# Kernel optimization log

Measured on AMD Instinct MI355X. Metric: run time of the kernel, lower is better.

The kernel has to match this reference:

```python
import jax, jax.numpy as jnp
import numpy as np

B, H, W, C = 4, 64, 64, 1280
NH = 16          # num heads
HD = C // NH     # 80 features per head
WS = 14          # window size
REL = 2 * WS - 1 # 27 relative-position entries per axis
EPS = 1e-6


def setup_inputs() -> dict:
    key = jax.random.key(0)
    ks = jax.random.split(key, 16)
    s = 0.02
    return {
        "imagelike_bhwc": jax.random.normal(ks[0], (B, H, W, C), jnp.float32),
        "ln1_g": jnp.ones((C,), jnp.float32),
        "ln1_b": jnp.zeros((C,), jnp.float32),
        "qkv_w": jax.random.normal(ks[1], (C, 3 * C), jnp.float32) * s,
        "qkv_b": jnp.zeros((3 * C,), jnp.float32),
        "proj_w": jax.random.normal(ks[2], (C, C), jnp.float32) * s,
        "proj_b": jnp.zeros((C,), jnp.float32),
        "rel_pos_h": jax.random.normal(ks[3], (REL, HD), jnp.float32) * s,
        "rel_pos_w": jax.random.normal(ks[4], (REL, HD), jnp.float32) * s,
        "ln2_g": jnp.ones((C,), jnp.float32),
        "ln2_b": jnp.zeros((C,), jnp.float32),
        "mlp_w1": jax.random.normal(ks[5], (C, 4 * C), jnp.float32) * s,
        "mlp_b1": jnp.zeros((4 * C,), jnp.float32),
        "mlp_w2": jax.random.normal(ks[6], (4 * C, C), jnp.float32) * s,
        "mlp_b2": jnp.zeros((C,), jnp.float32),
    }


def _layernorm(t, g, b):
    mu = jnp.mean(t, axis=-1, keepdims=True)
    var = jnp.var(t, axis=-1, keepdims=True)
    return (t - mu) * jax.lax.rsqrt(var + EPS) * g + b


def reference(imagelike_bhwc, ln1_g, ln1_b, qkv_w, qkv_b, proj_w, proj_b,
              rel_pos_h, rel_pos_w, ln2_g, ln2_b, mlp_w1, mlp_b1, mlp_w2, mlp_b2):
    x = imagelike_bhwc
    b, h, w, c = x.shape
    hd = c // NH
    scale = hd ** -0.5
    # --- image -> windows (pad to multiple of WS) ---
    hp, wp = (-h) % WS, (-w) % WS
    xp = jnp.pad(x, ((0, 0), (0, hp), (0, wp), (0, 0)))
    Hp, Wp = h + hp, w + wp
    ny, nx = Hp // WS, Wp // WS
    win = xp.reshape(b, ny, WS, nx, WS, c).transpose(0, 1, 3, 2, 4, 5)
    win = win.reshape(b * ny * nx, WS, WS, c)      # (Bw, S, S, C)
    Bw, N = win.shape[0], WS * WS
    # --- pre-attention layernorm + qkv ---
    t = _layernorm(win, ln1_g, ln1_b)
    qkv = t.reshape(Bw, N, c) @ qkv_w + qkv_b      # (Bw, N, 3C)
    qkv = qkv.reshape(Bw, N, 3, NH, hd).transpose(2, 0, 3, 1, 4)  # (3,Bw,NH,N,hd)
    q, k, v = qkv[0], qkv[1], qkv[2]
    # --- scores + decomposed relative position bias ---
    attn = jnp.einsum('bhqd,bhkd->bhqk', q * scale, k)            # (Bw,NH,N,N)
    idx = jnp.arange(WS)[:, None] - jnp.arange(WS)[None, :] + (WS - 1)
    Rh = rel_pos_h[idx]                                           # (WS,WS,hd)
    Rw = rel_pos_w[idx]                                           # (WS,WS,hd)
    qr = q.reshape(Bw, NH, WS, WS, hd)
    bias_h = jnp.einsum('bnyxd,ykd->bnyxk', qr, Rh)               # (Bw,NH,WS,WS,WS)
    bias_w = jnp.einsum('bnyxd,xkd->bnyxk', qr, Rw)
    bias = (bias_h[..., :, None] + bias_w[..., None, :]).reshape(Bw, NH, N, N)
    attn = jax.nn.softmax(attn + bias, axis=-1)
    out = jnp.einsum('bhqk,bhkd->bhqd', attn, v)                  # (Bw,NH,N,hd)
    out = out.transpose(0, 2, 1, 3).reshape(Bw, WS, WS, c)
    out = out @ proj_w + proj_b
    attn_out = out + win                                          # residual 1
    # --- MLP ---
    t2 = _layernorm(attn_out, ln2_g, ln2_b)
    mlp = jax.nn.gelu(t2 @ mlp_w1 + mlp_b1, approximate=False) @ mlp_w2 + mlp_b2
    out = mlp + attn_out                                          # residual 2
    # --- windows -> image (remove padding) ---
    img = out.reshape(b, ny, nx, WS, WS, c).transpose(0, 1, 3, 2, 4, 5)
    img = img.reshape(b, Hp, Wp, c)
    return img[:, :h, :w, :]
```

## Files before the change

kernel.cpp:

```cpp
#include <hip/hip_runtime.h>

typedef __attribute__((ext_vector_type(8))) short short8;
typedef __attribute__((ext_vector_type(4))) float f32x4;

#define GLBP(p) ((const __attribute__((address_space(1))) void*)(p))
#define LDSP(p) ((__attribute__((address_space(3))) void*)(p))

__device__ __forceinline__ float bf2f(unsigned short u) {
  return __uint_as_float(((unsigned int)u) << 16);
}
__device__ __forceinline__ unsigned short f2bf(float f) {
  unsigned int u = __float_as_uint(f);
  u += 0x7fff + ((u >> 16) & 1);
  return (unsigned short)(u >> 16);
}

__device__ __forceinline__ void tok2pix(int gt, int& b, int& py, int& px) {
  int w = gt / 196, t = gt - w * 196;
  b = w / 25;
  int wr = w - b * 25;
  int wy = wr / 5, wx = wr - wy * 5;
  int ty = t / 14;
  py = wy * 14 + ty;
  px = wx * 14 + (t - ty * 14);
}

__global__ void k_transpose(const float* __restrict__ W, unsigned short* __restrict__ Wt,
                            int K, int N) {
  __shared__ float tile[32][33];
  int tx = threadIdx.x, ty = threadIdx.y;
  int n0 = blockIdx.x * 32, k0 = blockIdx.y * 32;
#pragma unroll
  for (int i = 0; i < 4; ++i)
    tile[ty + 8 * i][tx] = W[(size_t)(k0 + ty + 8 * i) * N + n0 + tx];
  __syncthreads();
#pragma unroll
  for (int i = 0; i < 4; ++i)
    Wt[(size_t)(n0 + ty + 8 * i) * K + k0 + tx] = f2bf(tile[tx][ty + 8 * i]);
}

__global__ __launch_bounds__(256) void k_ln1(const float* __restrict__ x,
                                             const float* __restrict__ g,
                                             const float* __restrict__ be,
                                             unsigned short* __restrict__ A1,
                                             int w0, int ctok) {
  int m = blockIdx.x, tid = threadIdx.x;
  int b, py, px;
  tok2pix(w0 * 196 + m, b, py, px);
  bool valid = (m < ctok) && (py < 64) && (px < 64);
  const float* row = x + ((size_t)((b * 64 + py) * 64 + px)) * 1280;
  float v[5];
#pragma unroll
  for (int i = 0; i < 5; ++i) v[i] = valid ? row[tid + 256 * i] : 0.f;
  float s = 0.f, ss = 0.f;
#pragma unroll
  for (int i = 0; i < 5; ++i) { s += v[i]; ss += v[i] * v[i]; }
#pragma unroll
  for (int o = 32; o > 0; o >>= 1) { s += __shfl_down(s, o); ss += __shfl_down(ss, o); }
  __shared__ float rs[8];
  int wid = tid >> 6, lane = tid & 63;
  if (lane == 0) { rs[wid] = s; rs[wid + 4] = ss; }
  __syncthreads();
  s = rs[0] + rs[1] + rs[2] + rs[3];
  ss = rs[4] + rs[5] + rs[6] + rs[7];
  float mu = s * (1.f / 1280.f);
  float var = ss * (1.f / 1280.f) - mu * mu;
  float rinv = rsqrtf(var + 1e-6f);
  unsigned short* o1 = A1 + (size_t)m * 1280;
#pragma unroll
  for (int i = 0; i < 5; ++i) {
    int c = tid + 256 * i;
    o1[c] = f2bf((v[i] - mu) * rinv * g[c] + be[c]);
  }
}

__global__ __launch_bounds__(256) void k_ln2(const unsigned short* __restrict__ AT,
                                             const float* __restrict__ g,
                                             const float* __restrict__ be,
                                             unsigned short* __restrict__ A2) {
  int m = blockIdx.x, tid = threadIdx.x;
  const unsigned short* row = AT + (size_t)m * 1280;
  float v[5];
#pragma unroll
  for (int i = 0; i < 5; ++i) v[i] = bf2f(row[tid + 256 * i]);
  float s = 0.f, ss = 0.f;
#pragma unroll
  for (int i = 0; i < 5; ++i) { s += v[i]; ss += v[i] * v[i]; }
#pragma unroll
  for (int o = 32; o > 0; o >>= 1) { s += __shfl_down(s, o); ss += __shfl_down(ss, o); }
  __shared__ float rs[8];
  int wid = tid >> 6, lane = tid & 63;
  if (lane == 0) { rs[wid] = s; rs[wid + 4] = ss; }
  __syncthreads();
  s = rs[0] + rs[1] + rs[2] + rs[3];
  ss = rs[4] + rs[5] + rs[6] + rs[7];
  float mu = s * (1.f / 1280.f);
  float var = ss * (1.f / 1280.f) - mu * mu;
  float rinv = rsqrtf(var + 1e-6f);
  unsigned short* o1 = A2 + (size_t)m * 1280;
#pragma unroll
  for (int i = 0; i < 5; ++i) {
    int c = tid + 256 * i;
    o1[c] = f2bf((v[i] - mu) * rinv * g[c] + be[c]);
  }
}

template <int EPI>
__global__ __launch_bounds__(512, 2) void k_gemm256(const unsigned short* __restrict__ A,
                                                    const unsigned short* __restrict__ Bt,
                                                    int K, int N, int gx,
                                                    const float* __restrict__ bias,
                                                    void* __restrict__ outp,
                                                    const float* __restrict__ xres,
                                                    const unsigned short* __restrict__ attnres,
                                                    int w0, int ctok) {
  __shared__ __align__(16) char smem[131072];
  int tid = threadIdx.x;
  int w = tid >> 6, lane = tid & 63;
  int nwg = gridDim.x, bid = blockIdx.x;
  int q = nwg >> 3, r = nwg & 7;
  int xcd = bid & 7, loc = bid >> 3;
  int wg = (xcd < r ? xcd * (q + 1) : r * (q + 1) + (xcd - r) * q) + loc;
  int bx = wg % gx, by = wg / gx;
  int mBase = by * 256, nBase = bx * 256;
  int wr = w >> 2, wc = w & 3;
  int la = lane & 15, lg = lane >> 4;

  int rS = w * 16 + (lane >> 2);
  int kbyte = (((lane & 3) ^ ((lane >> 3) & 3)) << 4);
  const char* Ab = (const char*)A;
  const char* Bb = (const char*)Bt;
  const char* pa0 = Ab + ((size_t)(mBase + rS) * K) * 2 + kbyte;
  const char* pa1 = Ab + ((size_t)(mBase + 128 + rS) * K) * 2 + kbyte;
  const char* pb0 = Bb + ((size_t)(nBase + rS) * K) * 2 + kbyte;
  const char* pb1 = Bb + ((size_t)(nBase + 128 + rS) * K) * 2 + kbyte;
  int ldsw = w * 1024;

  auto STAGE = [&](int t) {
    int b = (t & 3) * 32768;
    size_t ko = (size_t)t * 64;
    __builtin_amdgcn_global_load_lds(GLBP(pa0 + ko), LDSP(smem + b + ldsw), 16, 0, 0);
    __builtin_amdgcn_global_load_lds(GLBP(pa1 + ko), LDSP(smem + b + 8192 + ldsw), 16, 0, 0);
    __builtin_amdgcn_global_load_lds(GLBP(pb0 + ko), LDSP(smem + b + 16384 + ldsw), 16, 0, 0);
    __builtin_amdgcn_global_load_lds(GLBP(pb1 + ko), LDSP(smem + b + 24576 + ldsw), 16, 0, 0);
  };

  int swz = ((lg ^ ((la >> 1) & 3)) << 4);
  int offA[8], offB[4];
#pragma unroll
  for (int m = 0; m < 8; ++m) offA[m] = (wr * 128 + m * 16 + la) * 64 + swz;
#pragma unroll
  for (int n = 0; n < 4; ++n) offB[n] = (wc * 64 + n * 16 + la) * 64 + swz;

  const f32x4 z4 = {0.f, 0.f, 0.f, 0.f};
  f32x4 acc[8][4];
#pragma unroll
  for (int m = 0; m < 8; ++m)
#pragma unroll
    for (int n = 0; n < 4; ++n) acc[m][n] = z4;

  int NT = K >> 5;
  STAGE(0);
  STAGE(1);
  STAGE(2);
  for (int t = 0; t < NT; ++t) {
    int rem = NT - 1 - t;
    if (rem >= 2)
      asm volatile("s_waitcnt vmcnt(8)" ::: "memory");
    else if (rem == 1)
      asm volatile("s_waitcnt vmcnt(4)" ::: "memory");
    else
      asm volatile("s_waitcnt vmcnt(0)" ::: "memory");
    __builtin_amdgcn_s_barrier();
    __builtin_amdgcn_sched_barrier(0);
    const char* buf = (const char*)smem + (t & 3) * 32768;
    short8 af[8], bfr[4];
#pragma unroll
    for (int m = 0; m < 4; ++m) af[m] = *(const short8*)(buf + offA[m]);
#pragma unroll
    for (int n = 0; n < 4; ++n) bfr[n] = *(const short8*)(buf + 16384 + offB[n]);
    if (t + 3 < NT) STAGE(t + 3);
    __builtin_amdgcn_s_setprio(1);
#pragma unroll
    for (int m = 0; m < 4; ++m)
#pragma unroll
      for (int n = 0; n < 4; ++n)
        acc[m][n] = __builtin_amdgcn_mfma_f32_16x16x32_bf16(af[m], bfr[n], acc[m][n], 0, 0, 0);
    __builtin_amdgcn_s_setprio(0);
    __builtin_amdgcn_s_barrier();
    __builtin_amdgcn_sched_barrier(0);
#pragma unroll
    for (int m = 4; m < 8; ++m) af[m] = *(const short8*)(buf + offA[m]);
    __builtin_amdgcn_s_setprio(1);
#pragma unroll
    for (int m = 4; m < 8; ++m)
#pragma unroll
      for (int n = 0; n < 4; ++n)
        acc[m][n] = __builtin_amdgcn_mfma_f32_16x16x32_bf16(af[m], bfr[n], acc[m][n], 0, 0, 0);
    __builtin_amdgcn_s_setprio(0);
  }

#pragma unroll
  for (int m = 0; m < 8; ++m) {
#pragma unroll
    for (int n = 0; n < 4; ++n) {
      int col = nBase + wc * 64 + n * 16 + la;
      float bcol = bias[col];
#pragma unroll
      for (int j = 0; j < 4; ++j) {
        int row = mBase + wr * 128 + m * 16 + lg * 4 + j;
        float v = acc[m][n][j] + bcol;
        if (EPI == 0) {
          ((unsigned short*)outp)[(size_t)row * N + col] = f2bf(v);
        } else if (EPI == 2) {
          float gg = 0.5f * v * (1.f + erff(v * 0.70710678118654752f));
          ((unsigned short*)outp)[(size_t)row * N + col] = f2bf(gg);
        } else if (EPI == 1) {
          if (row < ctok) {
            int b, py, px;
            tok2pix(w0 * 196 + row, b, py, px);
            float wv = (py < 64 && px < 64)
                           ? xres[((size_t)((b * 64 + py) * 64 + px)) * 1280 + col]
                           : 0.f;
            ((unsigned short*)outp)[(size_t)row * 1280 + col] = f2bf(v + wv);
          }
        } else {
          if (row < ctok) {
            int b, py, px;
            tok2pix(w0 * 196 + row, b, py, px);
            if (py < 64 && px < 64)
              ((float*)outp)[((size_t)((b * 64 + py) * 64 + px)) * 1280 + col] =
                  v + bf2f(attnres[(size_t)row * 1280 + col]);
          }
        }
      }
    }
  }
}

__global__ __launch_bounds__(256) void k_relbias(const unsigned short* __restrict__ qkv,
                                                 const float* __restrict__ rph,
                                                 const float* __restrict__ rpw,
                                                 unsigned short* __restrict__ B) {
  int wh = blockIdx.x;
  int w = wh >> 4, nh = wh & 15;
  const unsigned short* qb = qkv + (size_t)w * 196 * 3840 + nh * 80;
  for (int id = threadIdx.x; id < 196 * 28; id += 256) {
    int t = id / 28, which = id - t * 28;
    int y = t / 14, xx = t - y * 14;
    const float* R = (which < 14) ? (rph + (size_t)(y - which + 13) * 80)
                                  : (rpw + (size_t)(xx - (which - 14) + 13) * 80);
    const unsigned short* q = qb + (size_t)t * 3840;
    float acc = 0.f;
#pragma unroll
    for (int d8 = 0; d8 < 10; ++d8) {
      short8 qv = *(const short8*)(q + d8 * 8);
      const float4* Rv = (const float4*)(R + d8 * 8);
      float4 ra = Rv[0], rb = Rv[1];
      acc += bf2f((unsigned short)qv[0]) * ra.x + bf2f((unsigned short)qv[1]) * ra.y +
             bf2f((unsigned short)qv[2]) * ra.z + bf2f((unsigned short)qv[3]) * ra.w +
             bf2f((unsigned short)qv[4]) * rb.x + bf2f((unsigned short)qv[5]) * rb.y +
             bf2f((unsigned short)qv[6]) * rb.z + bf2f((unsigned short)qv[7]) * rb.w;
    }
    B[(size_t)wh * (196 * 28) + id] = f2bf(acc);
  }
}

__global__ __launch_bounds__(512) void k_attn(const unsigned short* __restrict__ qkv,
                                              const unsigned short* __restrict__ Bias,
                                              unsigned short* __restrict__ AO) {
  __shared__ unsigned short Ks[208 * 104];
  __shared__ unsigned short Vt[80 * 248];
  __shared__ unsigned short Ps[8][16 * 248];
  __shared__ unsigned short Bls[196 * 28];
  int wh = blockIdx.x;
  int w = wh >> 4, nh = wh & 15;
  int tid = threadIdx.x, wid = tid >> 6, lane = tid & 63;
  int la = lane & 15, lg = lane >> 4;
  const unsigned short* base = qkv + (size_t)w * 196 * 3840 + nh * 80;
  const short8 z8 = {0, 0, 0, 0, 0, 0, 0, 0};

  for (int c = tid; c < 208 * 13; c += 512) {
    int t = c / 13, seg = c - t * 13;
    short8 kv = z8;
    if (t < 196 && seg < 10) kv = *(const short8*)(base + (size_t)t * 3840 + 1280 + seg * 8);
    *(short8*)(Ks + t * 104 + seg * 8) = kv;
  }
  for (int c = tid; c < 28 * 80; c += 512) {
    int d = c % 80, tb = c / 80;
    short8 pk;
#pragma unroll
    for (int e = 0; e < 8; ++e) {
      int t = tb * 8 + e;
      pk[e] = (t < 196) ? (short)base[(size_t)t * 3840 + 2560 + d] : (short)0;
    }
    *(short8*)(Vt + d * 248 + tb * 8) = pk;
  }
  for (int i = tid; i < 196 * 28; i += 512) Bls[i] = Bias[(size_t)wh * (196 * 28) + i];
  __syncthreads();

  int kyv[13], kxv[13];
#pragma unroll
  for (int ci = 0; ci < 13; ++ci) {
    int key = ci * 16 + la;
    kyv[ci] = key / 14;
    kxv[ci] = key - kyv[ci] * 14;
  }

  const float scale = 0.111803398874989485f;
  const f32x4 z4 = {0.f, 0.f, 0.f, 0.f};
  unsigned short* P = Ps[wid];

  auto process = [&](int rb) {
    short8 qa[3];
#pragma unroll
    for (int kk = 0; kk < 3; ++kk) {
      int t = rb * 16 + la;
      int d = kk * 32 + lg * 8;
      qa[kk] = (t < 196 && d < 80) ? *(const short8*)(base + (size_t)t * 3840 + d) : z8;
    }
    f32x4 s[13];
#pragma unroll
    for (int i = 0; i < 13; ++i) s[i] = z4;
#pragma unroll
    for (int kk = 0; kk < 3; ++kk) {
#pragma unroll
      for (int ni = 0; ni < 13; ++ni) {
        short8 bb = *(const short8*)(Ks + (ni * 16 + la) * 104 + kk * 32 + lg * 8);
        s[ni] = __builtin_amdgcn_mfma_f32_16x16x32_bf16(qa[kk], bb, s[ni], 0, 0, 0);
      }
    }
#pragma unroll
    for (int j = 0; j < 4; ++j) {
      int rloc = lg * 4 + j;
      int t = rb * 16 + rloc;
      bool tval = t < 196;
      const unsigned short* Bp = Bls + (tval ? t : 0) * 28;
      float v[13];
      float mx = -3e30f;
#pragma unroll
      for (int ci = 0; ci < 13; ++ci) {
        int key = ci * 16 + la;
        float val = s[ci][j] * scale;
        if (key < 196 && tval) val += bf2f(Bp[kyv[ci]]) + bf2f(Bp[14 + kxv[ci]]);
        if (key >= 196) val = -3e30f;
        v[ci] = val;
        mx = fmaxf(mx, val);
      }
#pragma unroll
      for (int o = 1; o < 16; o <<= 1) mx = fmaxf(mx, __shfl_xor(mx, o));
      float sum = 0.f;
#pragma unroll
      for (int ci = 0; ci < 13; ++ci) {
        float e = __expf(v[ci] - mx);
        v[ci] = e;
        sum += e;
      }
#pragma unroll
      for (int o = 1; o < 16; o <<= 1) sum += __shfl_xor(sum, o);
      float inv = 1.f / sum;
#pragma unroll
      for (int ci = 0; ci < 13; ++ci) P[rloc * 248 + ci * 16 + la] = f2bf(v[ci] * inv);
      P[rloc * 248 + 208 + la] = 0;
    }
    f32x4 o5[5];
#pragma unroll
    for (int i = 0; i < 5; ++i) o5[i] = z4;
#pragma unroll
    for (int kc = 0; kc < 7; ++kc) {
      short8 a = *(const short8*)(P + la * 248 + kc * 32 + lg * 8);
#pragma unroll
      for (int ni = 0; ni < 5; ++ni) {
        short8 bb = *(const short8*)(Vt + (ni * 16 + la) * 248 + kc * 32 + lg * 8);
        o5[ni] = __builtin_amdgcn_mfma_f32_16x16x32_bf16(a, bb, o5[ni], 0, 0, 0);
      }
    }
#pragma unroll
    for (int ni = 0; ni < 5; ++ni)
#pragma unroll
      for (int j = 0; j < 4; ++j) {
        int t = rb * 16 + lg * 4 + j;
        if (t < 196)
          AO[((size_t)w * 196 + t) * 1280 + nh * 80 + ni * 16 + la] = f2bf(o5[ni][j]);
      }
  };

  process(wid);
  if (wid < 5) process(wid + 8);
}

extern "C" void kernel_launch(void* const* d_in, const int* in_sizes, int n_in,
                              void* d_out, int out_size, void* d_ws, size_t ws_size,
                              hipStream_t stream) {
  const float* x = (const float*)d_in[0];
  const float* ln1g = (const float*)d_in[1];
  const float* ln1b = (const float*)d_in[2];
  const float* qkvw = (const float*)d_in[3];
  const float* qkvb = (const float*)d_in[4];
  const float* projw = (const float*)d_in[5];
  const float* projb = (const float*)d_in[6];
  const float* rph = (const float*)d_in[7];
  const float* rpw = (const float*)d_in[8];
  const float* ln2g = (const float*)d_in[9];
  const float* ln2b = (const float*)d_in[10];
  const float* w1 = (const float*)d_in[11];
  const float* b1 = (const float*)d_in[12];
  const float* w2 = (const float*)d_in[13];
  const float* b2 = (const float*)d_in[14];
  float* out = (float*)d_out;

  const size_t woff = (3840ull * 1280 + 1280ull * 1280 + 5120ull * 1280 + 1280ull * 5120) * 2;
  const int NWopts[7] = {100, 50, 25, 10, 5, 2, 1};
  int NW = 0, Mb = 0;
  for (int i = 0; i < 7; ++i) {
    int nw = NWopts[i];
    int mb = ((nw * 196 + 255) / 256) * 256;
    size_t tot = woff + (size_t)mb * 2560  + (size_t)mb * 7680  +
                 (size_t)mb * 2560  + (size_t)nw * 16 * 196 * 28 * 2  +
                 (size_t)mb * 2560 ;
    if (tot <= ws_size) { NW = nw; Mb = mb; break; }
  }
  if (!NW) return;

  char* p = (char*)d_ws;
  unsigned short* qkvwT = (unsigned short*)p; p += 3840ull * 1280 * 2;
  unsigned short* projwT = (unsigned short*)p; p += 1280ull * 1280 * 2;
  unsigned short* w1T = (unsigned short*)p; p += 5120ull * 1280 * 2;
  unsigned short* w2T = (unsigned short*)p; p += 1280ull * 5120 * 2;
  unsigned short* A1 = (unsigned short*)p; p += (size_t)Mb * 2560;
  unsigned short* QKV = (unsigned short*)p; p += (size_t)Mb * 7680;
  unsigned short* AO = (unsigned short*)p; p += (size_t)Mb * 2560;
  unsigned short* BIAS = (unsigned short*)p; p += (size_t)NW * 16 * 196 * 28 * 2;
  unsigned short* ATTN = (unsigned short*)p;
  unsigned short* Hb = QKV;
  unsigned short* A2 = A1;

  k_transpose<<<dim3(120, 40), dim3(32, 8), 0, stream>>>(qkvw, qkvwT, 1280, 3840);
  k_transpose<<<dim3(40, 40), dim3(32, 8), 0, stream>>>(projw, projwT, 1280, 1280);
  k_transpose<<<dim3(160, 40), dim3(32, 8), 0, stream>>>(w1, w1T, 1280, 5120);
  k_transpose<<<dim3(40, 160), dim3(32, 8), 0, stream>>>(w2, w2T, 5120, 1280);

  int gy = Mb / 256;
  int nchunks = (100 + NW - 1) / NW;
  for (int c = 0; c < nchunks; ++c) {
    int w0 = c * NW;
    int cw = (100 - w0 < NW) ? (100 - w0) : NW;
    int ctok = cw * 196;
    k_ln1<<<Mb, 256, 0, stream>>>(x, ln1g, ln1b, A1, w0, ctok);
    k_gemm256<0><<<15 * gy, 512, 0, stream>>>(A1, qkvwT, 1280, 3840, 15, qkvb, (void*)QKV,
                                              nullptr, nullptr, 0, 0);
    k_relbias<<<cw * 16, 256, 0, stream>>>(QKV, rph, rpw, BIAS);
    k_attn<<<cw * 16, 512, 0, stream>>>(QKV, BIAS, AO);
    k_gemm256<1><<<5 * gy, 512, 0, stream>>>(AO, projwT, 1280, 1280, 5, projb, (void*)ATTN,
                                             x, nullptr, w0, ctok);
    k_ln2<<<Mb, 256, 0, stream>>>(ATTN, ln2g, ln2b, A2);
    k_gemm256<2><<<20 * gy, 512, 0, stream>>>(A2, w1T, 1280, 5120, 20, b1, (void*)Hb,
                                              nullptr, nullptr, 0, 0);
    k_gemm256<3><<<5 * gy, 512, 0, stream>>>(Hb, w2T, 5120, 1280, 5, b2, (void*)out,
                                             nullptr, ATTN, w0, ctok);
  }
}
```

Before: 1.730 ms.

## Retile GEMMs to 256x128 with BK=64 triple buffering, warp-per-row layernorm

The GEMM tile shrinks from 256x256 with K-step 32 to 256x128 with K-step 64, using a three-stage LDS ring, an XOR swizzle, one fewer barrier per iteration, and twice as many workgroups. Layernorm kernels now process four rows per block with one wavefront per row, replacing LDS reduction and __syncthreads with shuffles. The attention V transpose now uses vectorized global loads with scattered LDS stores. The GEMM template is wrapped in four named kernels. The aims are better CU occupancy and load balance and lower sync overhead, at the cost of less data reuse per tile and more LDS per block.

```diff
diff --git a/kernel.cpp b/kernel.cpp
--- a/kernel.cpp
+++ b/kernel.cpp
@@ -44,32 +44,29 @@
                                              const float* __restrict__ be,
                                              unsigned short* __restrict__ A1,
                                              int w0, int ctok) {
-  int m = blockIdx.x, tid = threadIdx.x;
+  int m = blockIdx.x * 4 + (threadIdx.x >> 6);
+  int lane = threadIdx.x & 63;
   int b, py, px;
   tok2pix(w0 * 196 + m, b, py, px);
   bool valid = (m < ctok) && (py < 64) && (px < 64);
   const float* row = x + ((size_t)((b * 64 + py) * 64 + px)) * 1280;
-  float v[5];
-#pragma unroll
-  for (int i = 0; i < 5; ++i) v[i] = valid ? row[tid + 256 * i] : 0.f;
+  float v[20];
+#pragma unroll
+  for (int i = 0; i < 20; ++i) v[i] = valid ? row[lane + 64 * i] : 0.f;
   float s = 0.f, ss = 0.f;
 #pragma unroll
-  for (int i = 0; i < 5; ++i) { s += v[i]; ss += v[i] * v[i]; }
+  for (int i = 0; i < 20; ++i) { s += v[i]; ss += v[i] * v[i]; }
 #pragma unroll
   for (int o = 32; o > 0; o >>= 1) { s += __shfl_down(s, o); ss += __shfl_down(ss, o); }
-  __shared__ float rs[8];
-  int wid = tid >> 6, lane = tid & 63;
-  if (lane == 0) { rs[wid] = s; rs[wid + 4] = ss; }
-  __syncthreads();
-  s = rs[0] + rs[1] + rs[2] + rs[3];
-  ss = rs[4] + rs[5] + rs[6] + rs[7];
+  s = __shfl(s, 0);
+  ss = __shfl(ss, 0);
   float mu = s * (1.f / 1280.f);
   float var = ss * (1.f / 1280.f) - mu * mu;
   float rinv = rsqrtf(var + 1e-6f);
   unsigned short* o1 = A1 + (size_t)m * 1280;
 #pragma unroll
-  for (int i = 0; i < 5; ++i) {
-    int c = tid + 256 * i;
+  for (int i = 0; i < 20; ++i) {
+    int c = lane + 64 * i;
     o1[c] = f2bf((v[i] - mu) * rinv * g[c] + be[c]);
   }
 }
@@ -78,43 +75,40 @@
                                              const float* __restrict__ g,
                                              const float* __restrict__ be,
                                              unsigned short* __restrict__ A2) {
-  int m = blockIdx.x, tid = threadIdx.x;
+  int m = blockIdx.x * 4 + (threadIdx.x >> 6);
+  int lane = threadIdx.x & 63;
   const unsigned short* row = AT + (size_t)m * 1280;
-  float v[5];
-#pragma unroll
-  for (int i = 0; i < 5; ++i) v[i] = bf2f(row[tid + 256 * i]);
+  float v[20];
+#pragma unroll
+  for (int i = 0; i < 20; ++i) v[i] = bf2f(row[lane + 64 * i]);
   float s = 0.f, ss = 0.f;
 #pragma unroll
-  for (int i = 0; i < 5; ++i) { s += v[i]; ss += v[i] * v[i]; }
+  for (int i = 0; i < 20; ++i) { s += v[i]; ss += v[i] * v[i]; }
 #pragma unroll
   for (int o = 32; o > 0; o >>= 1) { s += __shfl_down(s, o); ss += __shfl_down(ss, o); }
-  __shared__ float rs[8];
-  int wid = tid >> 6, lane = tid & 63;
-  if (lane == 0) { rs[wid] = s; rs[wid + 4] = ss; }
-  __syncthreads();
-  s = rs[0] + rs[1] + rs[2] + rs[3];
-  ss = rs[4] + rs[5] + rs[6] + rs[7];
+  s = __shfl(s, 0);
+  ss = __shfl(ss, 0);
   float mu = s * (1.f / 1280.f);
   float var = ss * (1.f / 1280.f) - mu * mu;
   float rinv = rsqrtf(var + 1e-6f);
   unsigned short* o1 = A2 + (size_t)m * 1280;
 #pragma unroll
-  for (int i = 0; i < 5; ++i) {
-    int c = tid + 256 * i;
+  for (int i = 0; i < 20; ++i) {
+    int c = lane + 64 * i;
     o1[c] = f2bf((v[i] - mu) * rinv * g[c] + be[c]);
   }
 }
 
 template <int EPI>
-__global__ __launch_bounds__(512, 2) void k_gemm256(const unsigned short* __restrict__ A,
-                                                    const unsigned short* __restrict__ Bt,
-                                                    int K, int N, int gx,
-                                                    const float* __restrict__ bias,
-                                                    void* __restrict__ outp,
-                                                    const float* __restrict__ xres,
-                                                    const unsigned short* __restrict__ attnres,
-                                                    int w0, int ctok) {
-  __shared__ __align__(16) char smem[131072];
+__device__ __forceinline__ void gemm_body(const unsigned short* __restrict__ A,
+                                          const unsigned short* __restrict__ Bt,
+                                          int K, int N, int gx,
+                                          const float* __restrict__ bias,
+                                          void* __restrict__ outp,
+                                          const float* __restrict__ xres,
+                                          const unsigned short* __restrict__ attnres,
+                                          int w0, int ctok) {
+  __shared__ __align__(16) char smem[147456];
   int tid = threadIdx.x;
   int w = tid >> 6, lane = tid & 63;
   int nwg = gridDim.x, bid = blockIdx.x;
@@ -122,89 +116,105 @@
   int xcd = bid & 7, loc = bid >> 3;
   int wg = (xcd < r ? xcd * (q + 1) : r * (q + 1) + (xcd - r) * q) + loc;
   int bx = wg % gx, by = wg / gx;
-  int mBase = by * 256, nBase = bx * 256;
+  int mBase = by * 256, nBase = bx * 128;
   int wr = w >> 2, wc = w & 3;
   int la = lane & 15, lg = lane >> 4;
 
-  int rS = w * 16 + (lane >> 2);
-  int kbyte = (((lane & 3) ^ ((lane >> 3) & 3)) << 4);
-  const char* Ab = (const char*)A;
-  const char* Bb = (const char*)Bt;
-  const char* pa0 = Ab + ((size_t)(mBase + rS) * K) * 2 + kbyte;
-  const char* pa1 = Ab + ((size_t)(mBase + 128 + rS) * K) * 2 + kbyte;
-  const char* pb0 = Bb + ((size_t)(nBase + rS) * K) * 2 + kbyte;
-  const char* pb1 = Bb + ((size_t)(nBase + 128 + rS) * K) * 2 + kbyte;
-  int ldsw = w * 1024;
-
-  auto STAGE = [&](int t) {
-    int b = (t & 3) * 32768;
-    size_t ko = (size_t)t * 64;
-    __builtin_amdgcn_global_load_lds(GLBP(pa0 + ko), LDSP(smem + b + ldsw), 16, 0, 0);
-    __builtin_amdgcn_global_load_lds(GLBP(pa1 + ko), LDSP(smem + b + 8192 + ldsw), 16, 0, 0);
-    __builtin_amdgcn_global_load_lds(GLBP(pb0 + ko), LDSP(smem + b + 16384 + ldsw), 16, 0, 0);
-    __builtin_amdgcn_global_load_lds(GLBP(pb1 + ko), LDSP(smem + b + 24576 + ldsw), 16, 0, 0);
+  int srow = tid >> 3;
+  int ssw = ((tid & 7) * 16) ^ ((srow & 7) << 4);
+  const char* pa[4];
+  const char* pb[2];
+#pragma unroll
+  for (int i = 0; i < 4; ++i)
+    pa[i] = (const char*)A + ((size_t)(mBase + srow + i * 64) * K) * 2 + ssw;
+#pragma unroll
+  for (int i = 0; i < 2; ++i)
+    pb[i] = (const char*)Bt + ((size_t)(nBase + srow + i * 64) * K) * 2 + ssw;
+  int ldst = tid * 16;
+
+  auto STAGE = [&](int sb, size_t ko) {
+#pragma unroll
+    for (int i = 0; i < 4; ++i)
+      __builtin_amdgcn_global_load_lds(GLBP(pa[i] + ko), LDSP(smem + sb + i * 8192 + ldst), 16, 0, 0);
+#pragma unroll
+    for (int i = 0; i < 2; ++i)
+      __builtin_amdgcn_global_load_lds(GLBP(pb[i] + ko), LDSP(smem + sb + 32768 + i * 8192 + ldst), 16, 0, 0);
   };
 
-  int swz = ((lg ^ ((la >> 1) & 3)) << 4);
-  int offA[8], offB[4];
-#pragma unroll
-  for (int m = 0; m < 8; ++m) offA[m] = (wr * 128 + m * 16 + la) * 64 + swz;
-#pragma unroll
-  for (int n = 0; n < 4; ++n) offB[n] = (wc * 64 + n * 16 + la) * 64 + swz;
+  int colk[2];
+#pragma unroll
+  for (int kk = 0; kk < 2; ++kk) colk[kk] = (kk * 64 + lg * 16) ^ ((la & 7) << 4);
+  int offA[8];
+#pragma unroll
+  for (int m = 0; m < 8; ++m) offA[m] = (wr * 128 + m * 16 + la) * 128;
+  int offB[2];
+#pragma unroll
+  for (int n = 0; n < 2; ++n) offB[n] = 32768 + (wc * 32 + n * 16 + la) * 128;
 
   const f32x4 z4 = {0.f, 0.f, 0.f, 0.f};
-  f32x4 acc[8][4];
+  f32x4 acc[8][2];
 #pragma unroll
   for (int m = 0; m < 8; ++m)
 #pragma unroll
-    for (int n = 0; n < 4; ++n) acc[m][n] = z4;
-
-  int NT = K >> 5;
-  STAGE(0);
-  STAGE(1);
-  STAGE(2);
+    for (int n = 0; n < 2; ++n) acc[m][n] = z4;
+
+  int NT = K >> 6;
+  STAGE(0, 0);
+  STAGE(49152, 128);
+  int rs = 0;
   for (int t = 0; t < NT; ++t) {
-    int rem = NT - 1 - t;
-    if (rem >= 2)
-      asm volatile("s_waitcnt vmcnt(8)" ::: "memory");
-    else if (rem == 1)
-      asm volatile("s_waitcnt vmcnt(4)" ::: "memory");
+    if (t + 1 < NT)
+      asm volatile("s_waitcnt vmcnt(6)" ::: "memory");
     else
       asm volatile("s_waitcnt vmcnt(0)" ::: "memory");
     __builtin_amdgcn_s_barrier();
     __builtin_amdgcn_sched_barrier(0);
-    const char* buf = (const char*)smem + (t & 3) * 32768;
-    short8 af[8], bfr[4];
-#pragma unroll
-    for (int m = 0; m < 4; ++m) af[m] = *(const short8*)(buf + offA[m]);
-#pragma unroll
-    for (int n = 0; n < 4; ++n) bfr[n] = *(const short8*)(buf + 16384 + offB[n]);
-    if (t + 3 < NT) STAGE(t + 3);
+    const char* buf = (const char*)smem + rs * 49152;
+    if (t + 2 < NT) {
+      int ws = rs + 2;
+      if (ws >= 3) ws -= 3;
+      STAGE(ws * 49152, (size_t)(t + 2) * 128);
+    }
+    short8 bfr[2][2], af[4][2];
+#pragma unroll
+    for (int n = 0; n < 2; ++n)
+#pragma unroll
+      for (int kk = 0; kk < 2; ++kk) bfr[n][kk] = *(const short8*)(buf + offB[n] + colk[kk]);
+#pragma unroll
+    for (int m = 0; m < 4; ++m)
+#pragma unroll
+      for (int kk = 0; kk < 2; ++kk) af[m][kk] = *(const short8*)(buf + offA[m] + colk[kk]);
     __builtin_amdgcn_s_setprio(1);
 #pragma unroll
     for (int m = 0; m < 4; ++m)
 #pragma unroll
-      for (int n = 0; n < 4; ++n)
-        acc[m][n] = __builtin_amdgcn_mfma_f32_16x16x32_bf16(af[m], bfr[n], acc[m][n], 0, 0, 0);
+      for (int n = 0; n < 2; ++n)
+#pragma unroll
+        for (int kk = 0; kk < 2; ++kk)
+          acc[m][n] = __builtin_amdgcn_mfma_f32_16x16x32_bf16(af[m][kk], bfr[n][kk], acc[m][n], 0, 0, 0);
     __builtin_amdgcn_s_setprio(0);
-    __builtin_amdgcn_s_barrier();
     __builtin_amdgcn_sched_barrier(0);
 #pragma unroll
-    for (int m = 4; m < 8; ++m) af[m] = *(const short8*)(buf + offA[m]);
+    for (int m = 0; m < 4; ++m)
+#pragma unroll
+      for (int kk = 0; kk < 2; ++kk) af[m][kk] = *(const short8*)(buf + offA[m + 4] + colk[kk]);
     __builtin_amdgcn_s_setprio(1);
 #pragma unroll
-    for (int m = 4; m < 8; ++m)
-#pragma unroll
-      for (int n = 0; n < 4; ++n)
-        acc[m][n] = __builtin_amdgcn_mfma_f32_16x16x32_bf16(af[m], bfr[n], acc[m][n], 0, 0, 0);
+    for (int m = 0; m < 4; ++m)
+#pragma unroll
+      for (int n = 0; n < 2; ++n)
+#pragma unroll
+        for (int kk = 0; kk < 2; ++kk)
+          acc[m + 4][n] = __builtin_amdgcn_mfma_f32_16x16x32_bf16(af[m][kk], bfr[n][kk], acc[m + 4][n], 0, 0, 0);
     __builtin_amdgcn_s_setprio(0);
+    rs = (rs == 2) ? 0 : rs + 1;
   }
 
 #pragma unroll
   for (int m = 0; m < 8; ++m) {
 #pragma unroll
-    for (int n = 0; n < 4; ++n) {
-      int col = nBase + wc * 64 + n * 16 + la;
+    for (int n = 0; n < 2; ++n) {
+      int col = nBase + wc * 32 + n * 16 + la;
       float bcol = bias[col];
 #pragma unroll
       for (int j = 0; j < 4; ++j) {
@@ -238,6 +248,27 @@
   }
 }
 
+__global__ __launch_bounds__(512, 2) void k_gqkv(const unsigned short* A, const unsigned short* Bt,
+                                                 int K, int N, int gx, const float* bias, void* o,
+                                                 const float* xr, const unsigned short* ar, int w0, int ct) {
+  gemm_body<0>(A, Bt, K, N, gx, bias, o, xr, ar, w0, ct);
+}
+__global__ __launch_bounds__(512, 2) void k_gproj(const unsigned short* A, const unsigned short* Bt,
+                                                  int K, int N, int gx, const float* bias, void* o,
+                                                  const float* xr, const unsigned short* ar, int w0, int ct) {
+  gemm_body<1>(A, Bt, K, N, gx, bias, o, xr, ar, w0, ct);
+}
+__global__ __launch_bounds__(512, 2) void k_gmlp1(const unsigned short* A, const unsigned short* Bt,
+                                                  int K, int N, int gx, const float* bias, void* o,
+                                                  const float* xr, const unsigned short* ar, int w0, int ct) {
+  gemm_body<2>(A, Bt, K, N, gx, bias, o, xr, ar, w0, ct);
+}
+__global__ __launch_bounds__(512, 2) void k_gmlp2(const unsigned short* A, const unsigned short* Bt,
+                                                  int K, int N, int gx, const float* bias, void* o,
+                                                  const float* xr, const unsigned short* ar, int w0, int ct) {
+  gemm_body<3>(A, Bt, K, N, gx, bias, o, xr, ar, w0, ct);
+}
+
 __global__ __launch_bounds__(256) void k_relbias(const unsigned short* __restrict__ qkv,
                                                  const float* __restrict__ rph,
                                                  const float* __restrict__ rpw,
@@ -250,11 +281,11 @@
     int y = t / 14, xx = t - y * 14;
     const float* R = (which < 14) ? (rph + (size_t)(y - which + 13) * 80)
                                   : (rpw + (size_t)(xx - (which - 14) + 13) * 80);
-    const unsigned short* q = qb + (size_t)t * 3840;
+    const unsigned short* qq = qb + (size_t)t * 3840;
     float acc = 0.f;
 #pragma unroll
     for (int d8 = 0; d8 < 10; ++d8) {
-      short8 qv = *(const short8*)(q + d8 * 8);
+      short8 qv = *(const short8*)(qq + d8 * 8);
       const float4* Rv = (const float4*)(R + d8 * 8);
       float4 ra = Rv[0], rb = Rv[1];
       acc += bf2f((unsigned short)qv[0]) * ra.x + bf2f((unsigned short)qv[1]) * ra.y +
@@ -286,16 +317,13 @@
     if (t < 196 && seg < 10) kv = *(const short8*)(base + (size_t)t * 3840 + 1280 + seg * 8);
     *(short8*)(Ks + t * 104 + seg * 8) = kv;
   }
-  for (int c = tid; c < 28 * 80; c += 512) {
-    int d = c % 80, tb = c / 80;
-    short8 pk;
-#pragma unroll
-    for (int e = 0; e < 8; ++e) {
-      int t = tb * 8 + e;
-      pk[e] = (t < 196) ? (short)base[(size_t)t * 3840 + 2560 + d] : (short)0;
-    }
-    *(short8*)(Vt + d * 248 + tb * 8) = pk;
-  }
+  for (int c = tid; c < 196 * 10; c += 512) {
+    int t = c / 10, d8 = (c - t * 10) * 8;
+    short8 vv = *(const short8*)(base + (size_t)t * 3840 + 2560 + d8);
+#pragma unroll
+    for (int e = 0; e < 8; ++e) Vt[(d8 + e) * 248 + t] = (unsigned short)vv[e];
+  }
+  for (int i = tid; i < 80 * 28; i += 512) Vt[(i / 28) * 248 + 196 + (i % 28)] = 0;
   for (int i = tid; i < 196 * 28; i += 512) Bls[i] = Bias[(size_t)wh * (196 * 28) + i];
   __syncthreads();
 
@@ -446,17 +474,17 @@
     int w0 = c * NW;
     int cw = (100 - w0 < NW) ? (100 - w0) : NW;
     int ctok = cw * 196;
-    k_ln1<<<Mb, 256, 0, stream>>>(x, ln1g, ln1b, A1, w0, ctok);
-    k_gemm256<0><<<15 * gy, 512, 0, stream>>>(A1, qkvwT, 1280, 3840, 15, qkvb, (void*)QKV,
-                                              nullptr, nullptr, 0, 0);
+    k_ln1<<<Mb / 4, 256, 0, stream>>>(x, ln1g, ln1b, A1, w0, ctok);
+    k_gqkv<<<30 * gy, 512, 0, stream>>>(A1, qkvwT, 1280, 3840, 30, qkvb, (void*)QKV,
+                                        nullptr, nullptr, 0, 0);
     k_relbias<<<cw * 16, 256, 0, stream>>>(QKV, rph, rpw, BIAS);
     k_attn<<<cw * 16, 512, 0, stream>>>(QKV, BIAS, AO);
-    k_gemm256<1><<<5 * gy, 512, 0, stream>>>(AO, projwT, 1280, 1280, 5, projb, (void*)ATTN,
-                                             x, nullptr, w0, ctok);
-    k_ln2<<<Mb, 256, 0, stream>>>(ATTN, ln2g, ln2b, A2);
-    k_gemm256<2><<<20 * gy, 512, 0, stream>>>(A2, w1T, 1280, 5120, 20, b1, (void*)Hb,
-                                              nullptr, nullptr, 0, 0);
-    k_gemm256<3><<<5 * gy, 512, 0, stream>>>(Hb, w2T, 5120, 1280, 5, b2, (void*)out,
-                                             nullptr, ATTN, w0, ctok);
-  }
-}
+    k_gproj<<<10 * gy, 512, 0, stream>>>(AO, projwT, 1280, 1280, 10, projb, (void*)ATTN,
+                                         x, nullptr, w0, ctok);
+    k_ln2<<<Mb / 4, 256, 0, stream>>>(ATTN, ln2g, ln2b, A2);
+    k_gmlp1<<<40 * gy, 512, 0, stream>>>(A2, w1T, 1280, 5120, 40, b1, (void*)Hb,
+                                         nullptr, nullptr, 0, 0);
+    k_gmlp2<<<10 * gy, 512, 0, stream>>>(Hb, w2T, 5120, 1280, 10, b2, (void*)out,
+                                         nullptr, ATTN, w0, ctok);
+  }
+}
```

Measured after the change: 1.808 ms. +4.5%, slower.
